# Kernel tuning notes

Measured on AMD Instinct MI355X. Metric: run time of the kernel, lower is better.

## Reference

```python
import jax, jax.numpy as jnp
import numpy as np
from jax import lax

CONF_BIT = 8        # mantissa bits for block-floating-point
CONF_GROUP_SIZE = 36  # elements sharing one exponent


def bfp_quantize(x, bits=CONF_BIT, group_size=CONF_GROUP_SIZE):
    """Group-wise block-floating-point quantization (make_groups_tensor).
    Consecutive groups of `group_size` elements of the flattened tensor share
    the exponent of the group's max magnitude; mantissas are rounded to `bits` bits."""
    shape = x.shape
    flat = x.reshape(-1)
    n = flat.shape[0]
    pad = (-n) % group_size
    flat = jnp.pad(flat, (0, pad))
    g = flat.reshape(-1, group_size)
    max_abs = jnp.max(jnp.abs(g), axis=1, keepdims=True)
    # shared exponent = floor(log2(max|x|)); guard zero groups
    exp = jnp.floor(jnp.log2(jnp.where(max_abs > 0, max_abs, 1.0)))
    step = jnp.exp2(exp - (bits - 1))  # quantization step per group
    qmax = 2 ** (bits - 1) - 1
    q = jnp.clip(jnp.round(g / step), -(qmax + 1), qmax) * step
    q = jnp.where(max_abs > 0, q, 0.0)
    return q.reshape(-1)[:n].reshape(shape)


def setup_inputs() -> dict:
    key = jax.random.key(0)
    k1, k2, k3 = jax.random.split(key, 3)
    B, Cin, Cout, H, W, K = 32, 128, 128, 112, 112, 3
    x = jax.random.normal(k1, (B, Cin, H, W), dtype=jnp.float32)
    fan_in = Cin * K * K
    weight = jax.random.normal(k2, (Cout, Cin, K, K), dtype=jnp.float32) / np.sqrt(fan_in)
    bound = 1.0 / np.sqrt(fan_in)
    bias = jax.random.uniform(k3, (Cout,), dtype=jnp.float32, minval=-bound, maxval=bound)
    return {"x": x, "weight": weight, "bias": bias}


def reference(x, weight, bias):
    # BFP-quantize input and weight, then plain conv2d (stride=1, padding=1)
    xq = bfp_quantize(x)
    wq = bfp_quantize(weight)
    out = lax.conv_general_dilated(
        xq, wq,
        window_strides=(1, 1),
        padding=((1, 1), (1, 1)),
        dimension_numbers=("NCHW", "OIHW", "NCHW"),
    )
    return out + bias[None, :, None, None]
```

## Files before the change

### kernel.cpp

```cpp
#include <hip/hip_runtime.h>

typedef __attribute__((ext_vector_type(8))) short short8;
typedef __attribute__((ext_vector_type(4))) float f32x4;

#define NB     32
#define NC     128
#define HW     112
#define PLANE  12544
#define XTOT   51380224
#define NGX    1427229
#define PADW   114
#define PADPLANE 12996
#define XPAD_BYTES 106463232ULL
#define WG_OFF     XPAD_BYTES
#define SE_OFF     (XPAD_BYTES + 294912ULL)

__device__ __forceinline__ void gld_lds16(const void* g, void* l) {
  __builtin_amdgcn_global_load_lds(
      (__attribute__((address_space(1))) unsigned int*)g,
      (__attribute__((address_space(3))) unsigned int*)l, 16, 0, 0);
}

__device__ __forceinline__ float qmax4(float4 v, float m) {
  m = fmaxf(m, fabsf(v.x)); m = fmaxf(m, fabsf(v.y));
  m = fmaxf(m, fabsf(v.z)); m = fmaxf(m, fabsf(v.w));
  return m;
}

__device__ __forceinline__ int bfp_exp(float m) {
  int e = 0;
  if (m > 0.f) {
    e = (int)((__float_as_uint(m) >> 23) & 255) - 127;
    if (e < -100) e = -100;
  }
  return e;
}

__device__ __forceinline__ unsigned short bfp_q(float v, float inv, float st) {
  float qq = fminf(fmaxf(rintf(v * inv), -128.f), 127.f) * st;
  return (unsigned short)(__float_as_uint(qq) >> 16);
}

__global__ __launch_bounds__(256) void quant_step_x(const float* __restrict__ x,
                                                    signed char* __restrict__ se) {
  int g = blockIdx.x * 256 + threadIdx.x;
  if (g >= NGX) return;
  int base = g * 36;
  float m = 0.f;
  if (base + 36 <= XTOT) {
    const float4* p4 = (const float4*)(x + base);
#pragma unroll
    for (int j = 0; j < 9; ++j) m = qmax4(p4[j], m);
  } else {
    for (int i = base; i < XTOT; ++i) m = fmaxf(m, fabsf(x[i]));
  }
  se[g] = (signed char)bfp_exp(m);
}

__global__ __launch_bounds__(64) void quant_w_kernel(const float* __restrict__ w,
                                                     unsigned short* __restrict__ wg) {
  int g = blockIdx.x * 64 + threadIdx.x;
  if (g >= 4096) return;
  const float4* p4 = (const float4*)(w + g * 36);
  float4 v[9];
  float m = 0.f;
#pragma unroll
  for (int j = 0; j < 9; ++j) { v[j] = p4[j]; m = qmax4(v[j], m); }
  int e = bfp_exp(m);
  float inv = __uint_as_float((unsigned)(134 - e) << 23);
  float st  = __uint_as_float((unsigned)(120 + e) << 23);
#pragma unroll
  for (int j = 0; j < 9; ++j) {
    float tmp[4] = {v[j].x, v[j].y, v[j].z, v[j].w};
#pragma unroll
    for (int k = 0; k < 4; ++k) {
      int i = j * 4 + k;
      int f = g * 36 + i;
      int co = f / 1152;
      int rem = f % 1152;
      int ci = rem / 9;
      int rs = rem % 9;
      int stp = rs * 4 + (ci >> 5);
      wg[(stp * 128 + co) * 32 + (ci & 31)] = bfp_q(tmp[i & 3] * 0.f + tmp[k], inv, st);
    }
  }
}

__global__ __launch_bounds__(256) void border_zero(unsigned short* __restrict__ xpad) {
  int tid = blockIdx.x * 256 + threadIdx.x;
  if (tid >= NB * 452 * 16) return;
  int b = tid / (452 * 16);
  int r = tid % (452 * 16);
  int pos = r >> 4, cc = r & 15;
  int hp, wp;
  if (pos < 114)      { hp = 0;             wp = pos; }
  else if (pos < 228) { hp = 113;           wp = pos - 114; }
  else if (pos < 340) { hp = pos - 228 + 1; wp = 0; }
  else                { hp = pos - 340 + 1; wp = 113; }
  float4 z = make_float4(0.f, 0.f, 0.f, 0.f);
  *(float4*)&xpad[((size_t)((b * 114 + hp) * 114 + wp)) * 128 + cc * 8] = z;
}

__global__ __launch_bounds__(256) void quant_pad_x(const float* __restrict__ x,
                                                   const signed char* __restrict__ se,
                                                   unsigned short* __restrict__ xpad) {
  __shared__ unsigned short tile[32 * 128];
  int b = blockIdx.y;
  int p0 = blockIdx.x * 32;
  int t = threadIdx.x;
  int pq  = (t & 7) * 4;
  int ci0 = (t >> 3) * 4;
  unsigned short q[4][4];
#pragma unroll
  for (int i = 0; i < 4; ++i) {
    int ci = ci0 + i;
    int f = (b * 128 + ci) * PLANE + p0 + pq;
    float4 v = *(const float4*)(x + f);
    float vv[4] = {v.x, v.y, v.z, v.w};
#pragma unroll
    for (int j = 0; j < 4; ++j) {
      int e = se[(f + j) / 36];
      float inv = __uint_as_float((unsigned)(134 - e) << 23);
      float st  = __uint_as_float((unsigned)(120 + e) << 23);
      q[i][j] = bfp_q(vv[j], inv, st);
    }
  }
#pragma unroll
  for (int j = 0; j < 4; ++j)
    *(ushort4*)&tile[(pq + j) * 128 + ci0] = make_ushort4(q[0][j], q[1][j], q[2][j], q[3][j]);
  __syncthreads();
  int pl = t >> 3;
  int cc = t & 7;
  int p = p0 + pl;
  int h = p / 112, w = p % 112;
  float4 v0 = *(const float4*)&tile[pl * 128 + cc * 16];
  float4 v1 = *(const float4*)&tile[pl * 128 + cc * 16 + 8];
  size_t dst = ((size_t)((b * 114 + h + 1) * 114 + (w + 1))) * 128 + cc * 16;
  *(float4*)&xpad[dst]     = v0;
  *(float4*)&xpad[dst + 8] = v1;
}

__global__ __launch_bounds__(256) void conv_mfma(const unsigned short* __restrict__ xpad,
                                                 const unsigned short* __restrict__ wg,
                                                 const float* __restrict__ bias,
                                                 float* __restrict__ out) {
  __shared__ unsigned short smem[8192];
  char* smb = (char*)smem;
  const int t = threadIdx.x;
  const int lane = t & 63, wv = t >> 6;
  const int lane15 = lane & 15, quad = lane >> 4;
  const int wm = wv >> 1, wn = wv & 1;
  const int b = blockIdx.y;
  const int p0 = blockIdx.x * 128;

  int a_src[2], b_src[2];
#pragma unroll
  for (int i = 0; i < 2; ++i) {
    int idx = t + i * 256;
    int row = idx >> 2;
    int c = idx & 3;
    int sw = (row >> 1) & 3;
    a_src[i] = row * 32 + (c ^ sw) * 8;
    int p = p0 + row;
    int h = p / 112, ww = p % 112;
    b_src[i] = ((b * 114 + h) * 114 + ww) * 128 + (c ^ sw) * 8;
  }

  int a_off[4], b_off[4];
#pragma unroll
  for (int f = 0; f < 4; ++f) {
    int row = wm * 64 + f * 16 + lane15;
    a_off[f] = row * 64 + ((quad ^ ((row >> 1) & 3)) * 16);
    int prow = wn * 64 + f * 16 + lane15;
    b_off[f] = 8192 + prow * 64 + ((quad ^ ((prow >> 1) & 3)) * 16);
  }

  f32x4 acc[4][4];
  f32x4 zero = {0.f, 0.f, 0.f, 0.f};
#pragma unroll
  for (int i = 0; i < 4; ++i)
#pragma unroll
    for (int j = 0; j < 4; ++j) acc[i][j] = zero;

  for (int step = 0; step < 36; ++step) {
    int rs = step >> 2, cib = step & 3;
    int r = rs / 3, s = rs % 3;
    int aofs = step * 4096;
    int bofs = (r * 114 + s) * 128 + cib * 32;
    __syncthreads();
#pragma unroll
    for (int i = 0; i < 2; ++i) {
      gld_lds16(wg + aofs + a_src[i],   smb + wv * 1024 + i * 4096);
      gld_lds16(xpad + b_src[i] + bofs, smb + 8192 + wv * 1024 + i * 4096);
    }
    __syncthreads();
    short8 af[4], bf[4];
#pragma unroll
    for (int f = 0; f < 4; ++f) af[f] = *(const short8*)(smb + a_off[f]);
#pragma unroll
    for (int f = 0; f < 4; ++f) bf[f] = *(const short8*)(smb + b_off[f]);
#pragma unroll
    for (int i = 0; i < 4; ++i)
#pragma unroll
      for (int j = 0; j < 4; ++j)
        acc[i][j] = __builtin_amdgcn_mfma_f32_16x16x32_bf16(af[i], bf[j], acc[i][j], 0, 0, 0);
  }

#pragma unroll
  for (int i = 0; i < 4; ++i)
#pragma unroll
    for (int j = 0; j < 4; ++j) {
      int p = p0 + wn * 64 + j * 16 + lane15;
#pragma unroll
      for (int rr = 0; rr < 4; ++rr) {
        int co = wm * 64 + i * 16 + quad * 4 + rr;
        out[(b * 128 + co) * PLANE + p] = acc[i][j][rr] + bias[co];
      }
    }
}

extern "C" void kernel_launch(void* const* d_in, const int* in_sizes, int n_in,
                              void* d_out, int out_size, void* d_ws, size_t ws_size,
                              hipStream_t stream) {
  const float* x    = (const float*)d_in[0];
  const float* w    = (const float*)d_in[1];
  const float* bias = (const float*)d_in[2];
  float* out = (float*)d_out;
  char* ws = (char*)d_ws;
  unsigned short* xpad = (unsigned short*)ws;
  unsigned short* wg   = (unsigned short*)(ws + WG_OFF);
  signed char*    se   = (signed char*)(ws + SE_OFF);

  quant_step_x<<<(NGX + 255) / 256, 256, 0, stream>>>(x, se);
  quant_w_kernel<<<64, 64, 0, stream>>>(w, wg);
  border_zero<<<904, 256, 0, stream>>>(xpad);
  quant_pad_x<<<dim3(392, 32), 256, 0, stream>>>(x, se, xpad);
  conv_mfma<<<dim3(98, 32), 256, 0, stream>>>(xpad, wg, bias, out);
}
```

Before: 556.1 us.

## Coalesce quantization passes and double conv K-chunk per LDS stage

The exponent pass now has each block load contiguous float4s into shared memory and reduce groups of 9 from there, so global reads are coalesced instead of strided 144-byte rows per thread. The pad/quantize kernel reads x with per-pixel coalesced scalar loads and writes through an XOR-swizzled LDS tile into 64-pixel blocks. The conv kernel loads 64 input channels per stage (18 stages instead of 36) with a wider 8-way swizzle, halving barrier count at the cost of twice the LDS. The conv changes could affect occupancy, and the index math must stay consistent with the weight layout.

```diff
diff --git a/kernel.cpp b/kernel.cpp
--- a/kernel.cpp
+++ b/kernel.cpp
@@ -4,13 +4,9 @@
 typedef __attribute__((ext_vector_type(4))) float f32x4;
 
 #define NB     32
-#define NC     128
-#define HW     112
 #define PLANE  12544
 #define XTOT   51380224
 #define NGX    1427229
-#define PADW   114
-#define PADPLANE 12996
 #define XPAD_BYTES 106463232ULL
 #define WG_OFF     XPAD_BYTES
 #define SE_OFF     (XPAD_BYTES + 294912ULL)
@@ -36,25 +32,39 @@
   return e;
 }
 
-__device__ __forceinline__ unsigned short bfp_q(float v, float inv, float st) {
+__device__ __forceinline__ unsigned int bfp_q(float v, float inv, float st) {
   float qq = fminf(fmaxf(rintf(v * inv), -128.f), 127.f) * st;
-  return (unsigned short)(__float_as_uint(qq) >> 16);
+  return __float_as_uint(qq) >> 16;
 }
 
 __global__ __launch_bounds__(256) void quant_step_x(const float* __restrict__ x,
                                                     signed char* __restrict__ se) {
-  int g = blockIdx.x * 256 + threadIdx.x;
-  if (g >= NGX) return;
-  int base = g * 36;
-  float m = 0.f;
-  if (base + 36 <= XTOT) {
-    const float4* p4 = (const float4*)(x + base);
-#pragma unroll
-    for (int j = 0; j < 9; ++j) m = qmax4(p4[j], m);
-  } else {
-    for (int i = base; i < XTOT; ++i) m = fmaxf(m, fabsf(x[i]));
-  }
-  se[g] = (signed char)bfp_exp(m);
+  __shared__ float red[1008];
+  const long long base4 = (long long)blockIdx.x * 1008;
+  const int t = threadIdx.x;
+#pragma unroll
+  for (int i = 0; i < 4; ++i) {
+    int idx = t + i * 256;
+    if (idx < 1008) {
+      long long f4 = base4 + idx;
+      float m = 0.f;
+      if (f4 * 4 < XTOT) {
+        float4 v = *(const float4*)(x + f4 * 4);
+        m = qmax4(v, 0.f);
+      }
+      red[idx] = m;
+    }
+  }
+  __syncthreads();
+  if (t < 112) {
+    long long g = (long long)blockIdx.x * 112 + t;
+    if (g < NGX) {
+      float m = red[t * 9];
+#pragma unroll
+      for (int k = 1; k < 9; ++k) m = fmaxf(m, red[t * 9 + k]);
+      se[g] = (signed char)bfp_exp(m);
+    }
+  }
 }
 
 __global__ __launch_bounds__(64) void quant_w_kernel(const float* __restrict__ w,
@@ -74,14 +84,13 @@
     float tmp[4] = {v[j].x, v[j].y, v[j].z, v[j].w};
 #pragma unroll
     for (int k = 0; k < 4; ++k) {
-      int i = j * 4 + k;
-      int f = g * 36 + i;
+      int f = g * 36 + j * 4 + k;
       int co = f / 1152;
       int rem = f % 1152;
       int ci = rem / 9;
       int rs = rem % 9;
       int stp = rs * 4 + (ci >> 5);
-      wg[(stp * 128 + co) * 32 + (ci & 31)] = bfp_q(tmp[i & 3] * 0.f + tmp[k], inv, st);
+      wg[(stp * 128 + co) * 32 + (ci & 31)] = (unsigned short)bfp_q(tmp[k], inv, st);
     }
   }
 }
@@ -104,47 +113,57 @@
 __global__ __launch_bounds__(256) void quant_pad_x(const float* __restrict__ x,
                                                    const signed char* __restrict__ se,
                                                    unsigned short* __restrict__ xpad) {
-  __shared__ unsigned short tile[32 * 128];
-  int b = blockIdx.y;
-  int p0 = blockIdx.x * 32;
-  int t = threadIdx.x;
-  int pq  = (t & 7) * 4;
-  int ci0 = (t >> 3) * 4;
-  unsigned short q[4][4];
-#pragma unroll
-  for (int i = 0; i < 4; ++i) {
-    int ci = ci0 + i;
-    int f = (b * 128 + ci) * PLANE + p0 + pq;
-    float4 v = *(const float4*)(x + f);
-    float vv[4] = {v.x, v.y, v.z, v.w};
+  __shared__ unsigned short tile[64 * 128];
+  const int t = threadIdx.x;
+  const int b = blockIdx.y;
+  const int p0 = blockIdx.x * 64;
+  const int pl = t & 63;
+  const int p = p0 + pl;
+  const int cq = (t >> 6) * 4;
+  const unsigned planebase = (unsigned)(b * 128) * PLANE + p;
+
+#pragma unroll
+  for (int i = 0; i < 8; ++i) {
+    int ci0 = cq + 16 * i;
+    unsigned q[4];
 #pragma unroll
     for (int j = 0; j < 4; ++j) {
-      int e = se[(f + j) / 36];
+      unsigned f = planebase + (unsigned)(ci0 + j) * PLANE;
+      float v = x[f];
+      int e = se[f / 36u];
       float inv = __uint_as_float((unsigned)(134 - e) << 23);
       float st  = __uint_as_float((unsigned)(120 + e) << 23);
-      q[i][j] = bfp_q(vv[j], inv, st);
-    }
-  }
-#pragma unroll
-  for (int j = 0; j < 4; ++j)
-    *(ushort4*)&tile[(pq + j) * 128 + ci0] = make_ushort4(q[0][j], q[1][j], q[2][j], q[3][j]);
+      q[j] = bfp_q(v, inv, st);
+    }
+    int phys = (ci0 >> 2) ^ (pl & 31);
+    uint2 pk;
+    pk.x = q[0] | (q[1] << 16);
+    pk.y = q[2] | (q[3] << 16);
+    *(uint2*)&tile[pl * 128 + phys * 4] = pk;
+  }
   __syncthreads();
-  int pl = t >> 3;
-  int cc = t & 7;
-  int p = p0 + pl;
-  int h = p / 112, w = p % 112;
-  float4 v0 = *(const float4*)&tile[pl * 128 + cc * 16];
-  float4 v1 = *(const float4*)&tile[pl * 128 + cc * 16 + 8];
-  size_t dst = ((size_t)((b * 114 + h + 1) * 114 + (w + 1))) * 128 + cc * 16;
-  *(float4*)&xpad[dst]     = v0;
-  *(float4*)&xpad[dst + 8] = v1;
+#pragma unroll
+  for (int j = 0; j < 4; ++j) {
+    int pl2 = (t >> 4) + 16 * j;
+    int c = t & 15;
+    int m = pl2 & 31;
+    int ps = (2 * c) ^ m;
+    uint4 v = *(uint4*)&tile[pl2 * 128 + (ps & ~1) * 4];
+    uint4 o;
+    if (m & 1) { o.x = v.z; o.y = v.w; o.z = v.x; o.w = v.y; }
+    else       { o = v; }
+    int p2 = p0 + pl2;
+    int h = p2 / 112, w = p2 % 112;
+    size_t dst = ((size_t)((b * 114 + h + 1) * 114) + (w + 1)) * 128 + c * 8;
+    *(uint4*)&xpad[dst] = o;
+  }
 }
 
 __global__ __launch_bounds__(256) void conv_mfma(const unsigned short* __restrict__ xpad,
                                                  const unsigned short* __restrict__ wg,
                                                  const float* __restrict__ bias,
                                                  float* __restrict__ out) {
-  __shared__ unsigned short smem[8192];
+  __shared__ unsigned short smem[16384];
   char* smb = (char*)smem;
   const int t = threadIdx.x;
   const int lane = t & 63, wv = t >> 6;
@@ -153,26 +172,29 @@
   const int b = blockIdx.y;
   const int p0 = blockIdx.x * 128;
 
-  int a_src[2], b_src[2];
-#pragma unroll
-  for (int i = 0; i < 2; ++i) {
+  int a_src[4], b_src[4];
+#pragma unroll
+  for (int i = 0; i < 4; ++i) {
     int idx = t + i * 256;
-    int row = idx >> 2;
-    int c = idx & 3;
-    int sw = (row >> 1) & 3;
-    a_src[i] = row * 32 + (c ^ sw) * 8;
+    int row = idx >> 3;
+    int c = idx & 7;
+    int cl = c ^ ((row >> 1) & 7);
+    a_src[i] = row * 32 + (cl >> 2) * 4096 + (cl & 3) * 8;
     int p = p0 + row;
     int h = p / 112, ww = p % 112;
-    b_src[i] = ((b * 114 + h) * 114 + ww) * 128 + (c ^ sw) * 8;
-  }
-
-  int a_off[4], b_off[4];
+    b_src[i] = ((b * 114 + h) * 114 + ww) * 128 + cl * 8;
+  }
+
+  int a_off[4][2], b_off[4][2];
 #pragma unroll
   for (int f = 0; f < 4; ++f) {
-    int row = wm * 64 + f * 16 + lane15;
-    a_off[f] = row * 64 + ((quad ^ ((row >> 1) & 3)) * 16);
-    int prow = wn * 64 + f * 16 + lane15;
-    b_off[f] = 8192 + prow * 64 + ((quad ^ ((prow >> 1) & 3)) * 16);
+#pragma unroll
+    for (int kk = 0; kk < 2; ++kk) {
+      int row = wm * 64 + f * 16 + lane15;
+      a_off[f][kk] = row * 128 + (((kk * 4 + quad) ^ ((row >> 1) & 7)) * 16);
+      int prow = wn * 64 + f * 16 + lane15;
+      b_off[f][kk] = 16384 + prow * 128 + (((kk * 4 + quad) ^ ((prow >> 1) & 7)) * 16);
+    }
   }
 
   f32x4 acc[4][4];
@@ -182,28 +204,31 @@
 #pragma unroll
     for (int j = 0; j < 4; ++j) acc[i][j] = zero;
 
-  for (int step = 0; step < 36; ++step) {
-    int rs = step >> 2, cib = step & 3;
-    int r = rs / 3, s = rs % 3;
-    int aofs = step * 4096;
-    int bofs = (r * 114 + s) * 128 + cib * 32;
+  for (int stage = 0; stage < 18; ++stage) {
+    int rs = stage >> 1, half = stage & 1;
+    int r = rs / 3, s = rs - r * 3;
+    int aofs = (rs * 4 + half * 2) * 4096;
+    int bofs = (r * 114 + s) * 128 + half * 64;
     __syncthreads();
 #pragma unroll
-    for (int i = 0; i < 2; ++i) {
-      gld_lds16(wg + aofs + a_src[i],   smb + wv * 1024 + i * 4096);
-      gld_lds16(xpad + b_src[i] + bofs, smb + 8192 + wv * 1024 + i * 4096);
+    for (int i = 0; i < 4; ++i) {
+      gld_lds16(wg + aofs + a_src[i],   smb + t * 16 + i * 4096);
+      gld_lds16(xpad + bofs + b_src[i], smb + 16384 + t * 16 + i * 4096);
     }
     __syncthreads();
-    short8 af[4], bf[4];
-#pragma unroll
-    for (int f = 0; f < 4; ++f) af[f] = *(const short8*)(smb + a_off[f]);
-#pragma unroll
-    for (int f = 0; f < 4; ++f) bf[f] = *(const short8*)(smb + b_off[f]);
-#pragma unroll
-    for (int i = 0; i < 4; ++i)
-#pragma unroll
-      for (int j = 0; j < 4; ++j)
-        acc[i][j] = __builtin_amdgcn_mfma_f32_16x16x32_bf16(af[i], bf[j], acc[i][j], 0, 0, 0);
+#pragma unroll
+    for (int kk = 0; kk < 2; ++kk) {
+      short8 af[4], bf[4];
+#pragma unroll
+      for (int f = 0; f < 4; ++f) af[f] = *(const short8*)(smb + a_off[f][kk]);
+#pragma unroll
+      for (int f = 0; f < 4; ++f) bf[f] = *(const short8*)(smb + b_off[f][kk]);
+#pragma unroll
+      for (int i = 0; i < 4; ++i)
+#pragma unroll
+        for (int j = 0; j < 4; ++j)
+          acc[i][j] = __builtin_amdgcn_mfma_f32_16x16x32_bf16(af[i], bf[j], acc[i][j], 0, 0, 0);
+    }
   }
 
 #pragma unroll
@@ -231,9 +256,9 @@
   unsigned short* wg   = (unsigned short*)(ws + WG_OFF);
   signed char*    se   = (signed char*)(ws + SE_OFF);
 
-  quant_step_x<<<(NGX + 255) / 256, 256, 0, stream>>>(x, se);
+  quant_step_x<<<12744, 256, 0, stream>>>(x, se);
   quant_w_kernel<<<64, 64, 0, stream>>>(w, wg);
   border_zero<<<904, 256, 0, stream>>>(xpad);
-  quant_pad_x<<<dim3(392, 32), 256, 0, stream>>>(x, se, xpad);
+  quant_pad_x<<<dim3(196, 32), 256, 0, stream>>>(x, se, xpad);
   conv_mfma<<<dim3(98, 32), 256, 0, stream>>>(xpad, wg, bias, out);
 }
```

New measurement: 556.6 us. About the same (+0.1%).
